# Kernel optimization log

Hardware: AMD Instinct MI355X
Metric: run time of the kernel (lower is better)

The kernel has to match this reference:

```python
import jax, jax.numpy as jnp
import numpy as np

WINDOW_SIZE = 512
NUM_HEADS = 16
HIDDEN = 1024
HEAD_DIM = HIDDEN // NUM_HEADS
SCALING = HEAD_DIM ** (-0.5)


def sliding_window_mask(seq_len, window_size):
    # row i attends to cols j with i - w//2 <= j <= i + w//2 (clipped to bounds)
    i = jnp.arange(seq_len)[:, None]
    j = jnp.arange(seq_len)[None, :]
    half = window_size // 2
    return jnp.abs(i - j) <= half  # [S, S] bool


def setup_inputs() -> dict:
    key = jax.random.key(0)
    k0, k1, k2, k3, k4 = jax.random.split(key, 5)
    B, S = 2, 2048
    hidden_states = jax.random.normal(k0, (B, S, HIDDEN), dtype=jnp.float32)
    scale = 0.02
    Wq = jax.random.normal(k1, (HIDDEN, HIDDEN), dtype=jnp.float32) * scale
    Wk = jax.random.normal(k2, (HIDDEN, HIDDEN), dtype=jnp.float32) * scale
    Wv = jax.random.normal(k3, (HIDDEN, HIDDEN), dtype=jnp.float32) * scale
    Wo = jax.random.normal(k4, (HIDDEN, HIDDEN), dtype=jnp.float32) * scale
    return {"hidden_states": hidden_states, "Wq": Wq, "Wk": Wk, "Wv": Wv, "Wo": Wo}


def reference(hidden_states, Wq, Wk, Wv, Wo):
    B, S, _ = hidden_states.shape
    # nn.Linear(bias=False): y = x @ W.T
    def proj(x, W):
        y = jnp.einsum('bsh,oh->bso', x, W)
        return y.reshape(B, S, NUM_HEADS, HEAD_DIM).transpose(0, 2, 1, 3)  # [B,H,S,D]

    q = proj(hidden_states, Wq)
    k = proj(hidden_states, Wk)
    v = proj(hidden_states, Wv)

    mask = sliding_window_mask(S, WINDOW_SIZE)  # [S,S]
    scores = jnp.einsum('bhsd,bhtd->bhst', q, k) * SCALING  # [B,H,S,S]
    scores = jnp.where(mask[None, None], scores, -jnp.inf)
    attn = jax.nn.softmax(scores, axis=-1)
    out = jnp.einsum('bhst,bhtd->bhsd', attn, v)
    out = out.transpose(0, 2, 1, 3).reshape(B, S, HIDDEN)
    out = jnp.einsum('bsh,oh->bso', out, Wo)
    return out, attn
```

## Files before the change

kernel.cpp:

```cpp
#include <hip/hip_runtime.h>

typedef unsigned short u16;
typedef __attribute__((ext_vector_type(8))) __bf16 bf16x8;
typedef __attribute__((ext_vector_type(4))) float f32x4;

#define DEV __device__ __forceinline__
#define SEQ 2048
#define SWZ(r) ((((r) & 7)) ^ (((r) >> 3) & 7))

DEV void async16(void* lds, const void* gptr) {
  __builtin_amdgcn_global_load_lds(
      (const __attribute__((address_space(1))) unsigned int*)gptr,
      (__attribute__((address_space(3))) unsigned int*)lds, 16, 0, 0);
}

DEV u16 f2bf(float x) {
  unsigned u = __float_as_uint(x);
  return (u16)((u + 0x7fffu + ((u >> 16) & 1u)) >> 16);
}

DEV f32x4 mfma(bf16x8 a, bf16x8 b, f32x4 c) {
  return __builtin_amdgcn_mfma_f32_16x16x32_bf16(a, b, c, 0, 0, 0);
}

__global__ __launch_bounds__(256) void k_cvt_all(
    const float* __restrict__ hs, const float* __restrict__ wq,
    const float* __restrict__ wk, const float* __restrict__ wv,
    const float* __restrict__ wo, u16* __restrict__ X16,
    u16* __restrict__ W16) {
  int b = blockIdx.x;
  const float* src;
  u16* dst;
  int off;
  if (b < 4096) {
    src = hs;
    dst = X16;
    off = b * 1024;
  } else {
    int b2 = b - 4096;
    int w = b2 >> 10;
    src = (w == 0) ? wq : (w == 1) ? wk : (w == 2) ? wv : wo;
    dst = W16 + (size_t)w * 1048576;
    off = (b2 & 1023) * 1024;
  }
  int i = off + threadIdx.x * 4;
  float4 v = *(const float4*)(src + i);
  *(ushort4*)(dst + i) = make_ushort4(f2bf(v.x), f2bf(v.y), f2bf(v.z), f2bf(v.w));
}

DEV void gemm_mainloop_db(const u16* __restrict__ A, const u16* __restrict__ B,
                          int K, u16* As, u16* Bs, f32x4 (&acc)[4][4],
                          int tid) {
  const int wid = tid >> 6, lane = tid & 63;
  const int wm = wid >> 1, wn = wid & 1;
  const int quad = lane >> 4, l15 = lane & 15;
  const int r0 = tid >> 2, g0 = (tid & 3) ^ (r0 & 3);
  const int r1 = (tid + 256) >> 2, g1 = ((tid + 256) & 3) ^ (r1 & 3);

  auto stage = [&](int buf, int k0) {
    u16* a = As + buf * 4096;
    u16* b = Bs + buf * 4096;
    async16(a + wid * 512, A + (size_t)r0 * K + k0 + g0 * 8);
    async16(a + wid * 512 + 2048, A + (size_t)r1 * K + k0 + g1 * 8);
    async16(b + wid * 512, B + (size_t)r0 * K + k0 + g0 * 8);
    async16(b + wid * 512 + 2048, B + (size_t)r1 * K + k0 + g1 * 8);
  };
  stage(0, 0);
  const int nk = K >> 5;
  for (int t = 0; t < nk; ++t) {
    __syncthreads();
    if (t + 1 < nk) stage((t + 1) & 1, (t + 1) * 32);
    const u16* a = As + (t & 1) * 4096;
    const u16* b = Bs + (t & 1) * 4096;
    bf16x8 af[4], bf[4];
#pragma unroll
    for (int mt = 0; mt < 4; ++mt) {
      int row = wm * 64 + mt * 16 + l15;
      af[mt] = *(const bf16x8*)(a + row * 32 + (quad ^ (row & 3)) * 8);
    }
#pragma unroll
    for (int nt = 0; nt < 4; ++nt) {
      int row = wn * 64 + nt * 16 + l15;
      bf[nt] = *(const bf16x8*)(b + row * 32 + (quad ^ (row & 3)) * 8);
    }
#pragma unroll
    for (int mt = 0; mt < 4; ++mt)
#pragma unroll
      for (int nt = 0; nt < 4; ++nt)
        acc[mt][nt] = mfma(af[mt], bf[nt], acc[mt][nt]);
  }
}

__global__ __launch_bounds__(256) void k_gemm_qkv(
    const u16* __restrict__ X, const u16* __restrict__ Wq,
    const u16* __restrict__ Wk, const u16* __restrict__ Wv,
    u16* __restrict__ Q16, u16* __restrict__ K16, u16* __restrict__ V16) {
  __shared__ u16 As[2 * 4096], Bs[2 * 4096];
  const int tid = threadIdx.x;
  const int bm = blockIdx.x, bn = blockIdx.y, z = blockIdx.z;
  const u16* B = (z == 0) ? Wq : (z == 1) ? Wk : Wv;
  u16* dst = (z == 0) ? Q16 : (z == 1) ? K16 : V16;
  const float sc = (z == 0) ? 0.125f : 1.0f;
  f32x4 acc[4][4];
#pragma unroll
  for (int i = 0; i < 4; ++i)
#pragma unroll
    for (int j = 0; j < 4; ++j) acc[i][j] = (f32x4){0.f, 0.f, 0.f, 0.f};
  gemm_mainloop_db(X + (size_t)bm * 128 * 1024, B + (size_t)bn * 128 * 1024,
                   1024, As, Bs, acc, tid);
  const int wid = tid >> 6, lane = tid & 63;
  const int wm = wid >> 1, wn = wid & 1, quad = lane >> 4, l15 = lane & 15;
#pragma unroll
  for (int mt = 0; mt < 4; ++mt)
#pragma unroll
    for (int nt = 0; nt < 4; ++nt)
#pragma unroll
      for (int r = 0; r < 4; ++r) {
        int row = bm * 128 + wm * 64 + mt * 16 + quad * 4 + r;
        int col = bn * 128 + wn * 64 + nt * 16 + l15;
        int b = row >> 11, s = row & 2047, h = col >> 6, d = col & 63;
        int bh = b * 16 + h;
        dst[((size_t)bh * SEQ + s) * 64 + d] = f2bf(acc[mt][nt][r] * sc);
      }
}

__global__ __launch_bounds__(256) void k_gemm_out(const u16* __restrict__ A,
                                                  const u16* __restrict__ Bw,
                                                  float* __restrict__ out) {
  __shared__ u16 As[2 * 2048], Bs[2 * 4096];
  const int tid = threadIdx.x;
  const int wid = tid >> 6, lane = tid & 63;
  const int wm = wid >> 1, wn = wid & 1;
  const int quad = lane >> 4, l15 = lane & 15;
  const int rA = tid >> 2, gA = (tid & 3) ^ (rA & 3);
  const int r1 = (tid + 256) >> 2, g1 = ((tid + 256) & 3) ^ (r1 & 3);
  const u16* Ab = A + (size_t)blockIdx.x * 64 * 1024;
  const u16* Bb = Bw + (size_t)blockIdx.y * 128 * 1024;
  f32x4 acc[2][4];
#pragma unroll
  for (int i = 0; i < 2; ++i)
#pragma unroll
    for (int j = 0; j < 4; ++j) acc[i][j] = (f32x4){0.f, 0.f, 0.f, 0.f};

  auto stage = [&](int buf, int k0) {
    async16(As + buf * 2048 + wid * 512, Ab + (size_t)rA * 1024 + k0 + gA * 8);
    async16(Bs + buf * 4096 + wid * 512, Bb + (size_t)rA * 1024 + k0 + gA * 8);
    async16(Bs + buf * 4096 + wid * 512 + 2048,
            Bb + (size_t)r1 * 1024 + k0 + g1 * 8);
  };
  stage(0, 0);
  for (int t = 0; t < 32; ++t) {
    __syncthreads();
    if (t + 1 < 32) stage((t + 1) & 1, (t + 1) * 32);
    const u16* a = As + (t & 1) * 2048;
    const u16* b = Bs + (t & 1) * 4096;
    bf16x8 af[2], bf[4];
#pragma unroll
    for (int mt = 0; mt < 2; ++mt) {
      int row = wm * 32 + mt * 16 + l15;
      af[mt] = *(const bf16x8*)(a + row * 32 + (quad ^ (row & 3)) * 8);
    }
#pragma unroll
    for (int nt = 0; nt < 4; ++nt) {
      int row = wn * 64 + nt * 16 + l15;
      bf[nt] = *(const bf16x8*)(b + row * 32 + (quad ^ (row & 3)) * 8);
    }
#pragma unroll
    for (int mt = 0; mt < 2; ++mt)
#pragma unroll
      for (int nt = 0; nt < 4; ++nt)
        acc[mt][nt] = mfma(af[mt], bf[nt], acc[mt][nt]);
  }
#pragma unroll
  for (int mt = 0; mt < 2; ++mt)
#pragma unroll
    for (int nt = 0; nt < 4; ++nt)
#pragma unroll
      for (int r = 0; r < 4; ++r) {
        int row = blockIdx.x * 64 + wm * 32 + mt * 16 + quad * 4 + r;
        int col = blockIdx.y * 128 + wn * 64 + nt * 16 + l15;
        out[(size_t)row * 1024 + col] = acc[mt][nt][r];
      }
}

__global__ __launch_bounds__(256, 2) void k_attn(
    const u16* __restrict__ Q16, const u16* __restrict__ K16,
    const u16* __restrict__ V16, float* __restrict__ attn_out,
    u16* __restrict__ O16) {
  __shared__ u16 Qt[4096];
  __shared__ u16 Kt[2][4096];
  __shared__ u16 Vt[2][4096];
  __shared__ u16 P[2][64 * 72];
  __shared__ float rowsum[64];

  const int tid = threadIdx.x, wid = tid >> 6, lane = tid & 63;
  const int quad = lane >> 4, l15 = lane & 15;
  const int qbase = blockIdx.x * 64;
  const int bh = blockIdx.y;
  const int b = bh >> 4, h = bh & 15;
  const u16* Qb = Q16 + ((size_t)bh * SEQ + qbase) * 64;
  const u16* Kb = K16 + (size_t)bh * SEQ * 64;
  const u16* Vb = V16 + (size_t)bh * SEQ * 64;
  float* attn_b = attn_out + (size_t)bh * SEQ * SEQ;

  const int r0 = tid >> 3, g0 = (tid & 7) ^ SWZ(r0);
  const int r1 = r0 + 32, g1 = (tid & 7) ^ SWZ(r1);

  const int tlo = qbase >= 256 ? 0 : (256 - qbase) >> 6;
  const int thi_raw = (SEQ - 64 - qbase + 256) >> 6;
  const int thi = thi_raw > 8 ? 8 : thi_raw;

  async16(Qt + wid * 512, Qb + r0 * 64 + g0 * 8);
  async16(Qt + wid * 512 + 2048, Qb + (size_t)r1 * 64 + g1 * 8);
  {
    int jb = qbase - 256 + tlo * 64;
    u16* Kd = Kt[tlo & 1];
    u16* Vd = Vt[tlo & 1];
    async16(Kd + wid * 512, Kb + (size_t)(jb + r0) * 64 + g0 * 8);
    async16(Kd + wid * 512 + 2048, Kb + (size_t)(jb + r1) * 64 + g1 * 8);
    async16(Vd + wid * 512, Vb + (size_t)(jb + r0) * 64 + g0 * 8);
    async16(Vd + wid * 512 + 2048, Vb + (size_t)(jb + r1) * 64 + g1 * 8);
  }
  if (tid < 64) rowsum[tid] = 0.f;

  float racc[4][4];
  f32x4 oacc[4];
#pragma unroll
  for (int mt = 0; mt < 4; ++mt) {
    oacc[mt] = (f32x4){0.f, 0.f, 0.f, 0.f};
#pragma unroll
    for (int r = 0; r < 4; ++r) racc[mt][r] = 0.f;
  }
  unsigned stash[9][8];
  bf16x8 bv_prev[2];
  bf16x8 aq[4][2];
  bool aq_loaded = false;
  const int d = wid * 16 + l15;

#pragma unroll
  for (int t = 0; t < 9; ++t) {
    if (t < tlo || t > thi) continue;
    const int jbase = qbase - 256 + t * 64;
    __syncthreads();
    if (t < thi) {
      int jb = jbase + 64;
      u16* Kd = Kt[(t + 1) & 1];
      u16* Vd = Vt[(t + 1) & 1];
      async16(Kd + wid * 512, Kb + (size_t)(jb + r0) * 64 + g0 * 8);
      async16(Kd + wid * 512 + 2048, Kb + (size_t)(jb + r1) * 64 + g1 * 8);
      async16(Vd + wid * 512, Vb + (size_t)(jb + r0) * 64 + g0 * 8);
      async16(Vd + wid * 512 + 2048, Vb + (size_t)(jb + r1) * 64 + g1 * 8);
    }
    if (!aq_loaded) {
      aq_loaded = true;
#pragma unroll
      for (int mt = 0; mt < 4; ++mt)
#pragma unroll
        for (int ks = 0; ks < 2; ++ks) {
          int row = mt * 16 + l15;
          aq[mt][ks] = *(const bf16x8*)(Qt + row * 64 +
                                        (((ks * 4 + quad) ^ SWZ(row)) * 8));
        }
    }
    if (t > tlo) {
      const u16* Pp = P[(t + 1) & 1];
#pragma unroll
      for (int mt = 0; mt < 4; ++mt) {
        int row = mt * 16 + l15;
        bf16x8 ap0 = *(const bf16x8*)(Pp + row * 72 + quad * 8);
        bf16x8 ap1 = *(const bf16x8*)(Pp + row * 72 + 32 + quad * 8);
        oacc[mt] = mfma(ap0, bv_prev[0], oacc[mt]);
        oacc[mt] = mfma(ap1, bv_prev[1], oacc[mt]);
      }
    }
    const u16* Ktc = Kt[t & 1];
    const u16* Vtc = Vt[t & 1];
    bf16x8 bq[2];
#pragma unroll
    for (int ks = 0; ks < 2; ++ks) {
      int row = wid * 16 + l15;
      bq[ks] =
          *(const bf16x8*)(Ktc + row * 64 + (((ks * 4 + quad) ^ SWZ(row)) * 8));
    }
#pragma unroll
    for (int ks = 0; ks < 2; ++ks)
#pragma unroll
      for (int jj = 0; jj < 8; ++jj) {
        int j = ks * 32 + quad * 8 + jj;
        int slot = (d >> 3) ^ SWZ(j);
        bv_prev[ks][jj] = *(const __bf16*)(Vtc + j * 64 + slot * 8 + (d & 7));
      }
    u16* Pc = P[t & 1];
    const int jcol = jbase + wid * 16 + l15;
#pragma unroll
    for (int mt = 0; mt < 4; ++mt) {
      f32x4 c = (f32x4){0.f, 0.f, 0.f, 0.f};
      c = mfma(aq[mt][0], bq[0], c);
      c = mfma(aq[mt][1], bq[1], c);
      unsigned p0 = 0, p1 = 0;
#pragma unroll
      for (int r = 0; r < 4; ++r) {
        int i_ = qbase + mt * 16 + quad * 4 + r;
        int dlt = i_ - jcol;
        dlt = dlt < 0 ? -dlt : dlt;
        float e = 0.f;
        if (dlt <= 256) e = __expf(c[r]);
        racc[mt][r] += e;
        unsigned eb = f2bf(e);
        Pc[(mt * 16 + quad * 4 + r) * 72 + wid * 16 + l15] = (u16)eb;
        if (r == 0) p0 = eb;
        if (r == 1) p0 |= eb << 16;
        if (r == 2) p1 = eb;
        if (r == 3) p1 |= eb << 16;
      }
      stash[t][mt * 2] = p0;
      stash[t][mt * 2 + 1] = p1;
    }
  }
  __syncthreads();
  {
    const u16* Pp = P[thi & 1];
#pragma unroll
    for (int mt = 0; mt < 4; ++mt) {
      int row = mt * 16 + l15;
      bf16x8 ap0 = *(const bf16x8*)(Pp + row * 72 + quad * 8);
      bf16x8 ap1 = *(const bf16x8*)(Pp + row * 72 + 32 + quad * 8);
      oacc[mt] = mfma(ap0, bv_prev[0], oacc[mt]);
      oacc[mt] = mfma(ap1, bv_prev[1], oacc[mt]);
    }
  }

#pragma unroll
  for (int mt = 0; mt < 4; ++mt)
#pragma unroll
    for (int r = 0; r < 4; ++r) {
      float v = racc[mt][r];
      v += __shfl_xor(v, 1, 16);
      v += __shfl_xor(v, 2, 16);
      v += __shfl_xor(v, 4, 16);
      v += __shfl_xor(v, 8, 16);
      racc[mt][r] = v;
    }
  if (l15 == 0) {
#pragma unroll
    for (int mt = 0; mt < 4; ++mt)
#pragma unroll
      for (int r = 0; r < 4; ++r)
        atomicAdd(&rowsum[mt * 16 + quad * 4 + r], racc[mt][r]);
  }
  __syncthreads();
  float linv[4][4];
#pragma unroll
  for (int mt = 0; mt < 4; ++mt)
#pragma unroll
    for (int r = 0; r < 4; ++r)
      linv[mt][r] = 1.0f / rowsum[mt * 16 + quad * 4 + r];

#pragma unroll
  for (int mt = 0; mt < 4; ++mt)
#pragma unroll
    for (int r = 0; r < 4; ++r) {
      int i_ = qbase + mt * 16 + quad * 4 + r;
      O16[((size_t)b * SEQ + i_) * 1024 + h * 64 + d] =
          f2bf(oacc[mt][r] * linv[mt][r]);
    }

#pragma unroll
  for (int mt = 0; mt < 4; ++mt)
#pragma unroll
    for (int r = 0; r < 4; ++r) {
      int i_ = qbase + mt * 16 + quad * 4 + r;
      float* p = attn_b + (size_t)i_ * SEQ + (qbase - 256) + d;
#pragma unroll
      for (int t = 0; t < 9; ++t) {
        if (t < tlo || t > thi) continue;
        unsigned pk = stash[t][mt * 2 + (r >> 1)];
        unsigned bits = (r & 1) ? (pk & 0xffff0000u) : (pk << 16);
        __builtin_nontemporal_store(__uint_as_float(bits) * linv[mt][r],
                                    p + t * 64);
      }
    }
}

extern "C" void kernel_launch(void* const* d_in, const int* in_sizes, int n_in,
                              void* d_out, int out_size, void* d_ws,
                              size_t ws_size, hipStream_t stream) {
  const float* hs = (const float*)d_in[0];
  const float* Wq = (const float*)d_in[1];
  const float* Wk = (const float*)d_in[2];
  const float* Wv = (const float*)d_in[3];
  const float* Wo = (const float*)d_in[4];
  float* out = (float*)d_out;
  float* attn = out + (size_t)4194304;

  u16* X16 = (u16*)d_ws;
  u16* Wq16 = X16 + 4194304;
  u16* Wk16 = Wq16 + 1048576;
  u16* Wv16 = Wk16 + 1048576;
  u16* Wo16 = Wv16 + 1048576;
  u16* Q16 = Wo16 + 1048576;
  u16* K16 = Q16 + 4194304;
  u16* V16 = K16 + 4194304;
  u16* O16 = V16 + 4194304;

  k_cvt_all<<<8192, 256, 0, stream>>>(hs, Wq, Wk, Wv, Wo, X16, Wq16);
  k_gemm_qkv<<<dim3(32, 8, 3), 256, 0, stream>>>(X16, Wq16, Wk16, Wv16, Q16,
                                                 K16, V16);
  k_attn<<<dim3(32, 32), 256, 0, stream>>>(Q16, K16, V16, attn, O16);
  k_gemm_out<<<dim3(64, 8), 256, 0, stream>>>(O16, Wo16, out);
}
```

Baseline: 586.2 us.

## Store V transposed from QKV GEMM and stage attn-prob writes through LDS

The QKV projection now writes V in a transposed [bh, d, seq] layout by staging the tile through shared memory, so the attention kernel can load its V fragments with single 16-byte vector LDS reads instead of eight scalar bf16 gathers. The attention probability output is also staged through a shared float tile per key block, then written as row-contiguous 16-byte nontemporal stores instead of scattered 4-byte stores. This is meant to cut LDS instruction count and improve write coalescing for the large [B,H,S,S] attn output. The cost is extra __syncthreads and LDS traffic per tile in the epilogue, plus a larger shared-memory union.

```diff
diff --git a/kernel.cpp b/kernel.cpp
--- a/kernel.cpp
+++ b/kernel.cpp
@@ -94,12 +94,17 @@
 __global__ __launch_bounds__(256) void k_gemm_qkv(
     const u16* __restrict__ X, const u16* __restrict__ Wq,
     const u16* __restrict__ Wk, const u16* __restrict__ Wv,
-    u16* __restrict__ Q16, u16* __restrict__ K16, u16* __restrict__ V16) {
-  __shared__ u16 As[2 * 4096], Bs[2 * 4096];
+    u16* __restrict__ Q16, u16* __restrict__ K16, u16* __restrict__ Vt16) {
+  __shared__ union alignas(16) SU {
+    struct {
+      u16 As[2 * 4096];
+      u16 Bs[2 * 4096];
+    } ab;
+    u16 T[128 * 136];
+  } su;
   const int tid = threadIdx.x;
   const int bm = blockIdx.x, bn = blockIdx.y, z = blockIdx.z;
   const u16* B = (z == 0) ? Wq : (z == 1) ? Wk : Wv;
-  u16* dst = (z == 0) ? Q16 : (z == 1) ? K16 : V16;
   const float sc = (z == 0) ? 0.125f : 1.0f;
   f32x4 acc[4][4];
 #pragma unroll
@@ -107,21 +112,46 @@
 #pragma unroll
     for (int j = 0; j < 4; ++j) acc[i][j] = (f32x4){0.f, 0.f, 0.f, 0.f};
   gemm_mainloop_db(X + (size_t)bm * 128 * 1024, B + (size_t)bn * 128 * 1024,
-                   1024, As, Bs, acc, tid);
+                   1024, su.ab.As, su.ab.Bs, acc, tid);
   const int wid = tid >> 6, lane = tid & 63;
   const int wm = wid >> 1, wn = wid & 1, quad = lane >> 4, l15 = lane & 15;
-#pragma unroll
-  for (int mt = 0; mt < 4; ++mt)
-#pragma unroll
-    for (int nt = 0; nt < 4; ++nt)
-#pragma unroll
-      for (int r = 0; r < 4; ++r) {
-        int row = bm * 128 + wm * 64 + mt * 16 + quad * 4 + r;
-        int col = bn * 128 + wn * 64 + nt * 16 + l15;
-        int b = row >> 11, s = row & 2047, h = col >> 6, d = col & 63;
-        int bh = b * 16 + h;
-        dst[((size_t)bh * SEQ + s) * 64 + d] = f2bf(acc[mt][nt][r] * sc);
-      }
+  if (z != 2) {
+    u16* dst = (z == 0) ? Q16 : K16;
+#pragma unroll
+    for (int mt = 0; mt < 4; ++mt)
+#pragma unroll
+      for (int nt = 0; nt < 4; ++nt)
+#pragma unroll
+        for (int r = 0; r < 4; ++r) {
+          int row = bm * 128 + wm * 64 + mt * 16 + quad * 4 + r;
+          int col = bn * 128 + wn * 64 + nt * 16 + l15;
+          int b = row >> 11, s = row & 2047, h = col >> 6, d = col & 63;
+          int bh = b * 16 + h;
+          dst[((size_t)bh * SEQ + s) * 64 + d] = f2bf(acc[mt][nt][r] * sc);
+        }
+  } else {
+    __syncthreads();
+#pragma unroll
+    for (int mt = 0; mt < 4; ++mt)
+#pragma unroll
+      for (int nt = 0; nt < 4; ++nt)
+#pragma unroll
+        for (int r = 0; r < 4; ++r) {
+          int row = wm * 64 + mt * 16 + quad * 4 + r;
+          int col = wn * 64 + nt * 16 + l15;
+          su.T[col * 136 + row] = f2bf(acc[mt][nt][r]);
+        }
+    __syncthreads();
+    const int c = tid >> 1, half = tid & 1;
+    const int colg = bn * 128 + c;
+    const int hh = colg >> 6, dd = colg & 63;
+    const int bh = (bm >> 4) * 16 + hh;
+    u16* dp = Vt16 + ((size_t)bh * 64 + dd) * SEQ + (bm & 15) * 128 + half * 64;
+    const u16* sp = su.T + c * 136 + half * 64;
+#pragma unroll
+    for (int k = 0; k < 8; ++k)
+      *(uint4*)(dp + k * 8) = *(const uint4*)(sp + k * 8);
+  }
 }
 
 __global__ __launch_bounds__(256) void k_gemm_out(const u16* __restrict__ A,
@@ -185,12 +215,17 @@
 
 __global__ __launch_bounds__(256, 2) void k_attn(
     const u16* __restrict__ Q16, const u16* __restrict__ K16,
-    const u16* __restrict__ V16, float* __restrict__ attn_out,
+    const u16* __restrict__ Vt16, float* __restrict__ attn_out,
     u16* __restrict__ O16) {
-  __shared__ u16 Qt[4096];
-  __shared__ u16 Kt[2][4096];
-  __shared__ u16 Vt[2][4096];
-  __shared__ u16 P[2][64 * 72];
+  __shared__ union alignas(16) U {
+    struct {
+      u16 Qt[4096];
+      u16 Kt[2][4096];
+      u16 Vt[2][4096];
+      u16 P[2][64 * 72];
+    } s;
+    float Pf[64 * 68];
+  } sm;
   __shared__ float rowsum[64];
 
   const int tid = threadIdx.x, wid = tid >> 6, lane = tid & 63;
@@ -200,7 +235,7 @@
   const int b = bh >> 4, h = bh & 15;
   const u16* Qb = Q16 + ((size_t)bh * SEQ + qbase) * 64;
   const u16* Kb = K16 + (size_t)bh * SEQ * 64;
-  const u16* Vb = V16 + (size_t)bh * SEQ * 64;
+  const u16* Vb = Vt16 + (size_t)bh * 64 * SEQ;
   float* attn_b = attn_out + (size_t)bh * SEQ * SEQ;
 
   const int r0 = tid >> 3, g0 = (tid & 7) ^ SWZ(r0);
@@ -210,16 +245,16 @@
   const int thi_raw = (SEQ - 64 - qbase + 256) >> 6;
   const int thi = thi_raw > 8 ? 8 : thi_raw;
 
-  async16(Qt + wid * 512, Qb + r0 * 64 + g0 * 8);
-  async16(Qt + wid * 512 + 2048, Qb + (size_t)r1 * 64 + g1 * 8);
+  async16(sm.s.Qt + wid * 512, Qb + r0 * 64 + g0 * 8);
+  async16(sm.s.Qt + wid * 512 + 2048, Qb + (size_t)r1 * 64 + g1 * 8);
   {
     int jb = qbase - 256 + tlo * 64;
-    u16* Kd = Kt[tlo & 1];
-    u16* Vd = Vt[tlo & 1];
+    u16* Kd = sm.s.Kt[tlo & 1];
+    u16* Vd = sm.s.Vt[tlo & 1];
     async16(Kd + wid * 512, Kb + (size_t)(jb + r0) * 64 + g0 * 8);
     async16(Kd + wid * 512 + 2048, Kb + (size_t)(jb + r1) * 64 + g1 * 8);
-    async16(Vd + wid * 512, Vb + (size_t)(jb + r0) * 64 + g0 * 8);
-    async16(Vd + wid * 512 + 2048, Vb + (size_t)(jb + r1) * 64 + g1 * 8);
+    async16(Vd + wid * 512, Vb + (size_t)r0 * SEQ + jb + g0 * 8);
+    async16(Vd + wid * 512 + 2048, Vb + (size_t)r1 * SEQ + jb + g1 * 8);
   }
   if (tid < 64) rowsum[tid] = 0.f;
 
@@ -244,12 +279,12 @@
     __syncthreads();
     if (t < thi) {
       int jb = jbase + 64;
-      u16* Kd = Kt[(t + 1) & 1];
-      u16* Vd = Vt[(t + 1) & 1];
+      u16* Kd = sm.s.Kt[(t + 1) & 1];
+      u16* Vd = sm.s.Vt[(t + 1) & 1];
       async16(Kd + wid * 512, Kb + (size_t)(jb + r0) * 64 + g0 * 8);
       async16(Kd + wid * 512 + 2048, Kb + (size_t)(jb + r1) * 64 + g1 * 8);
-      async16(Vd + wid * 512, Vb + (size_t)(jb + r0) * 64 + g0 * 8);
-      async16(Vd + wid * 512 + 2048, Vb + (size_t)(jb + r1) * 64 + g1 * 8);
+      async16(Vd + wid * 512, Vb + (size_t)r0 * SEQ + jb + g0 * 8);
+      async16(Vd + wid * 512 + 2048, Vb + (size_t)r1 * SEQ + jb + g1 * 8);
     }
     if (!aq_loaded) {
       aq_loaded = true;
@@ -258,12 +293,12 @@
 #pragma unroll
         for (int ks = 0; ks < 2; ++ks) {
           int row = mt * 16 + l15;
-          aq[mt][ks] = *(const bf16x8*)(Qt + row * 64 +
+          aq[mt][ks] = *(const bf16x8*)(sm.s.Qt + row * 64 +
                                         (((ks * 4 + quad) ^ SWZ(row)) * 8));
         }
     }
     if (t > tlo) {
-      const u16* Pp = P[(t + 1) & 1];
+      const u16* Pp = sm.s.P[(t + 1) & 1];
 #pragma unroll
       for (int mt = 0; mt < 4; ++mt) {
         int row = mt * 16 + l15;
@@ -273,24 +308,17 @@
         oacc[mt] = mfma(ap1, bv_prev[1], oacc[mt]);
       }
     }
-    const u16* Ktc = Kt[t & 1];
-    const u16* Vtc = Vt[t & 1];
+    const u16* Ktc = sm.s.Kt[t & 1];
+    const u16* Vtc = sm.s.Vt[t & 1];
     bf16x8 bq[2];
 #pragma unroll
     for (int ks = 0; ks < 2; ++ks) {
       int row = wid * 16 + l15;
-      bq[ks] =
-          *(const bf16x8*)(Ktc + row * 64 + (((ks * 4 + quad) ^ SWZ(row)) * 8));
-    }
-#pragma unroll
-    for (int ks = 0; ks < 2; ++ks)
-#pragma unroll
-      for (int jj = 0; jj < 8; ++jj) {
-        int j = ks * 32 + quad * 8 + jj;
-        int slot = (d >> 3) ^ SWZ(j);
-        bv_prev[ks][jj] = *(const __bf16*)(Vtc + j * 64 + slot * 8 + (d & 7));
-      }
-    u16* Pc = P[t & 1];
+      int sw = ((ks * 4 + quad) ^ SWZ(row)) * 8;
+      bq[ks] = *(const bf16x8*)(Ktc + row * 64 + sw);
+      bv_prev[ks] = *(const bf16x8*)(Vtc + row * 64 + sw);
+    }
+    u16* Pc = sm.s.P[t & 1];
     const int jcol = jbase + wid * 16 + l15;
 #pragma unroll
     for (int mt = 0; mt < 4; ++mt) {
@@ -319,7 +347,7 @@
   }
   __syncthreads();
   {
-    const u16* Pp = P[thi & 1];
+    const u16* Pp = sm.s.P[thi & 1];
 #pragma unroll
     for (int mt = 0; mt < 4; ++mt) {
       int row = mt * 16 + l15;
@@ -365,21 +393,31 @@
           f2bf(oacc[mt][r] * linv[mt][r]);
     }
 
-#pragma unroll
-  for (int mt = 0; mt < 4; ++mt)
-#pragma unroll
-    for (int r = 0; r < 4; ++r) {
-      int i_ = qbase + mt * 16 + quad * 4 + r;
-      float* p = attn_b + (size_t)i_ * SEQ + (qbase - 256) + d;
-#pragma unroll
-      for (int t = 0; t < 9; ++t) {
-        if (t < tlo || t > thi) continue;
-        unsigned pk = stash[t][mt * 2 + (r >> 1)];
-        unsigned bits = (r & 1) ? (pk & 0xffff0000u) : (pk << 16);
-        __builtin_nontemporal_store(__uint_as_float(bits) * linv[mt][r],
-                                    p + t * 64);
-      }
-    }
+  const int wcol = (tid & 15) * 4, wrow = tid >> 4;
+#pragma unroll
+  for (int t = 0; t < 9; ++t) {
+    if (t < tlo || t > thi) continue;
+    const int jbase = qbase - 256 + t * 64;
+    __syncthreads();
+#pragma unroll
+    for (int mt = 0; mt < 4; ++mt) {
+      unsigned p0 = stash[t][mt * 2], p1 = stash[t][mt * 2 + 1];
+      int rb = mt * 16 + quad * 4;
+      int cc = wid * 16 + l15;
+      sm.Pf[(rb + 0) * 68 + cc] = __uint_as_float(p0 << 16) * linv[mt][0];
+      sm.Pf[(rb + 1) * 68 + cc] = __uint_as_float(p0 & 0xffff0000u) * linv[mt][1];
+      sm.Pf[(rb + 2) * 68 + cc] = __uint_as_float(p1 << 16) * linv[mt][2];
+      sm.Pf[(rb + 3) * 68 + cc] = __uint_as_float(p1 & 0xffff0000u) * linv[mt][3];
+    }
+    __syncthreads();
+#pragma unroll
+    for (int k = 0; k < 4; ++k) {
+      int row = wrow + k * 16;
+      f32x4 v = *(const f32x4*)(sm.Pf + row * 68 + wcol);
+      __builtin_nontemporal_store(
+          v, (f32x4*)(attn_b + (size_t)(qbase + row) * SEQ + jbase + wcol));
+    }
+  }
 }
 
 extern "C" void kernel_launch(void* const* d_in, const int* in_sizes, int n_in,
@@ -400,12 +438,12 @@
   u16* Wo16 = Wv16 + 1048576;
   u16* Q16 = Wo16 + 1048576;
   u16* K16 = Q16 + 4194304;
-  u16* V16 = K16 + 4194304;
-  u16* O16 = V16 + 4194304;
+  u16* Vt16 = K16 + 4194304;
+  u16* O16 = Vt16 + 4194304;
 
   k_cvt_all<<<8192, 256, 0, stream>>>(hs, Wq, Wk, Wv, Wo, X16, Wq16);
   k_gemm_qkv<<<dim3(32, 8, 3), 256, 0, stream>>>(X16, Wq16, Wk16, Wv16, Q16,
-                                                 K16, V16);
-  k_attn<<<dim3(32, 32), 256, 0, stream>>>(Q16, K16, V16, attn, O16);
+                                                 K16, Vt16);
+  k_attn<<<dim3(32, 32), 256, 0, stream>>>(Q16, K16, Vt16, attn, O16);
   k_gemm_out<<<dim3(64, 8), 256, 0, stream>>>(O16, Wo16, out);
 }
```

Result: no change. 584.7 us (-0.3%).
